# Optimization experiments

Measured on AMD Instinct MI355X. Metric: run time of the kernel, lower is better.

## Reference

```python
import jax, jax.numpy as jnp
import numpy as np

N = 100000   # nodes
E = 1600000  # edges
G = 256      # graphs in batch
IN = 128     # in_feats
H = 64       # h_feats


def _xavier(k, shape):
    fan_in, fan_out = shape
    lim = float(np.sqrt(6.0 / (fan_in + fan_out)))
    return jax.random.uniform(k, shape, jnp.float32, -lim, lim)


def setup_inputs() -> dict:
    key = jax.random.key(0)
    ks = jax.random.split(key, 12)
    x = jax.random.normal(ks[0], (N, IN), jnp.float32)
    src = jax.random.randint(ks[1], (E,), 0, N)
    dst = jax.random.randint(ks[2], (E,), 0, N)
    ew = jax.random.uniform(ks[3], (E,), jnp.float32)
    gid = jnp.sort(jax.random.randint(ks[4], (N,), 0, G))
    def lin(k, fi, fo):
        kw, kb = jax.random.split(k)
        lim = float(np.sqrt(1.0 / fi))
        return (jax.random.uniform(kw, (fi, fo), jnp.float32, -lim, lim),
                jax.random.uniform(kb, (fo,), jnp.float32, -lim, lim))
    W1 = _xavier(ks[5], (IN, H)); b1 = jnp.zeros((H,), jnp.float32)
    W2 = _xavier(ks[6], (H, H));  b2 = jnp.zeros((H,), jnp.float32)
    W3 = _xavier(ks[7], (H, H));  b3 = jnp.zeros((H,), jnp.float32)
    Dw1, Db1 = lin(ks[8], H, 16)
    Dw2, Db2 = lin(ks[9], 16, 8)
    Dw3, Db3 = lin(ks[10], 8, 1)
    return {"x": x, "src": src, "dst": dst, "ew": ew, "gid": gid,
            "W1": W1, "b1": b1, "W2": W2, "b2": b2, "W3": W3, "b3": b3,
            "Dw1": Dw1, "Db1": Db1, "Dw2": Dw2, "Db2": Db2, "Dw3": Dw3, "Db3": Db3}


def reference(x, src, dst, ew, gid, W1, b1, W2, b2, W3, b3,
              Dw1, Db1, Dw2, Db2, Dw3, Db3):
    n = x.shape[0]
    # DGL GraphConv norm='both': unweighted degrees, clamped to >= 1
    deg_out = jnp.zeros((n,), x.dtype).at[src].add(1.0)
    deg_in = jnp.zeros((n,), x.dtype).at[dst].add(1.0)
    ns = jax.lax.rsqrt(jnp.maximum(deg_out, 1.0))  # src-side norm
    nd = jax.lax.rsqrt(jnp.maximum(deg_in, 1.0))   # dst-side norm

    def conv(h, W, b):
        # apply weight first (in >= out), then gather-scale-scatter
        h = (h * ns[:, None]) @ W                      # [N, out]
        m = h[src] * ew[:, None]                       # [E, out] edge messages
        agg = jnp.zeros((n, W.shape[1]), h.dtype).at[dst].add(m)
        return agg * nd[:, None] + b

    h = jax.nn.relu(conv(x, W1, b1))
    h = jax.nn.relu(conv(h, W2, b2))
    h = jax.nn.relu(conv(h, W3, b3))

    # mean_nodes: per-graph mean pooling
    counts = jnp.zeros((G,), h.dtype).at[gid].add(1.0)
    pooled = jnp.zeros((G, h.shape[1]), h.dtype).at[gid].add(h)
    pooled = pooled / jnp.maximum(counts, 1.0)[:, None]

    h = jax.nn.relu(pooled @ Dw1 + Db1)
    h = jax.nn.relu(h @ Dw2 + Db2)
    return jax.nn.sigmoid(h @ Dw3 + Db3)  # [G, 1]
```

## Files before the change

kernel.cpp:

```cpp
#include <hip/hip_runtime.h>
#include <math.h>

#define N_NODES 100000
#define N_EDGES 1600000
#define G_GRAPHS 256
#define IN_F 128
#define H_F 64

#define HB 40
#define HCHUNK (N_EDGES / HB)
#define NWORDS (N_NODES / 4)
#define HNODES 25000
#define HWORDS (HNODES / 4)
#define HR 4

#define NREG 160
#define REG_NODES 625
#define BUCKET_CAP 11000
#define BSPAN 6400
#define NB_BUCKET (N_EDGES / BSPAN)

typedef unsigned int uint_t;
typedef unsigned short ushort_t;
typedef unsigned char uchar_t;
typedef __attribute__((ext_vector_type(8))) short short8;
typedef __attribute__((ext_vector_type(4))) float floatx4;
typedef __attribute__((ext_vector_type(2))) float floatx2;

constexpr int WROW_F = H_F + 8;

__device__ __forceinline__ ushort_t f2bf(float f) {
  uint_t u = __float_as_uint(f);
  uint_t r = (u + 0x7fffu + ((u >> 16) & 1u)) >> 16;
  return (ushort_t)r;
}
__device__ __forceinline__ float bflo(uint_t u) { return __uint_as_float(u << 16); }
__device__ __forceinline__ uchar_t f2fp8(float f) {
  return (uchar_t)(__builtin_amdgcn_cvt_pk_fp8_f32(f, f, 0, false) & 0xff);
}

__global__ __launch_bounds__(256) void build_a_kernel(
    const int* __restrict__ src, const int* __restrict__ dst,
    const float* __restrict__ ew, int* __restrict__ bcnt,
    uint2* __restrict__ bucket, uint_t* __restrict__ p8src) {
  __shared__ uint_t shm[BSPAN + 2 * NREG];
  if (blockIdx.x < NB_BUCKET) {
    uint_t* rl = shm;
    int* cnt = (int*)(shm + BSPAN);
    int* cur = cnt + NREG;
    const int e0 = blockIdx.x * BSPAN;

    for (int i = threadIdx.x; i < NREG; i += 256) cnt[i] = 0;
    __syncthreads();

    for (int i = threadIdx.x; i < BSPAN; i += 256) {
      uint_t d = (uint_t)dst[e0 + i];
      uint_t r = d / REG_NODES;
      uint_t loc = d - r * REG_NODES;
      rl[i] = (r << 16) | loc;
      atomicAdd(&cnt[r], 1);
    }
    __syncthreads();

    for (int i = threadIdx.x; i < NREG; i += 256)
      cur[i] = atomicAdd(&bcnt[i], cnt[i]);
    __syncthreads();

    for (int i = threadIdx.x; i < BSPAN; i += 256) {
      uint_t v = rl[i];
      uint_t r = v >> 16, loc = v & 0xffffu;
      int pos = atomicAdd(&cur[r], 1);
      if (pos < BUCKET_CAP)
        bucket[(size_t)r * BUCKET_CAP + pos] = make_uint2(
            (loc << 17) | (uint_t)src[e0 + i], __float_as_uint(ew[e0 + i]));
    }
  } else {
    uint_t* h = shm;
    const int idx = blockIdx.x - NB_BUCKET;
    const int r = idx / HB;
    const int b = idx % HB;
    const uint_t rbase = (uint_t)(r * HNODES);

    for (int i = threadIdx.x; i < HWORDS; i += 256) h[i] = 0u;
    __syncthreads();

    const uint4* k4 = (const uint4*)(src + b * HCHUNK);
    for (int i = threadIdx.x; i < HCHUNK / 4; i += 256) {
      uint4 v = k4[i];
      uint_t t;
      t = v.x - rbase; if (t < (uint_t)HNODES) atomicAdd(&h[t >> 2], 1u << ((t & 3u) * 8u));
      t = v.y - rbase; if (t < (uint_t)HNODES) atomicAdd(&h[t >> 2], 1u << ((t & 3u) * 8u));
      t = v.z - rbase; if (t < (uint_t)HNODES) atomicAdd(&h[t >> 2], 1u << ((t & 3u) * 8u));
      t = v.w - rbase; if (t < (uint_t)HNODES) atomicAdd(&h[t >> 2], 1u << ((t & 3u) * 8u));
    }
    __syncthreads();

    uint_t* outp = p8src + (size_t)b * NWORDS + r * HWORDS;
    for (int i = threadIdx.x; i < HWORDS; i += 256) outp[i] = h[i];
  }
}

__global__ __launch_bounds__(1024) void build_b_kernel(
    const uint2* __restrict__ bucket, const int* __restrict__ bcnt,
    const uint_t* __restrict__ p8src, uint_t* __restrict__ csr,
    int2* __restrict__ rc, float* __restrict__ nd, float* __restrict__ ns) {
  __shared__ uint_t staged[BUCKET_CAP];
  __shared__ int cnt[REG_NODES];
  __shared__ int sc[REG_NODES];
  __shared__ int ts[1024];
  const int tid = threadIdx.x;
  if (blockIdx.x >= NREG) {
    int w = (blockIdx.x - NREG) * 1024 + tid;
    if (w >= NWORDS) return;
    int c0 = 0, c1 = 0, c2 = 0, c3 = 0;
    for (int b = 0; b < HB; ++b) {
      uint_t xv = p8src[(size_t)b * NWORDS + w];
      c0 += (int)(xv & 0xffu);
      c1 += (int)((xv >> 8) & 0xffu);
      c2 += (int)((xv >> 16) & 0xffu);
      c3 += (int)((xv >> 24) & 0xffu);
    }
    ((float4*)ns)[w] = make_float4(
        rsqrtf(fmaxf((float)c0, 1.0f)), rsqrtf(fmaxf((float)c1, 1.0f)),
        rsqrtf(fmaxf((float)c2, 1.0f)), rsqrtf(fmaxf((float)c3, 1.0f)));
    return;
  }
  const int r = blockIdx.x;
  const int nE = min(bcnt[r], BUCKET_CAP);

  ts[tid] = (tid < NREG) ? min(bcnt[tid], BUCKET_CAP) : 0;
  for (int i = tid; i < REG_NODES; i += 1024) cnt[i] = 0;
  __syncthreads();
  for (int off = 1; off < 256; off <<= 1) {
    int t = (tid >= off) ? ts[tid - off] : 0;
    __syncthreads();
    ts[tid] += t;
    __syncthreads();
  }
  const int csr_base = (r == 0) ? 0 : ts[r - 1];
  __syncthreads();

  const uint2* bk = bucket + (size_t)r * BUCKET_CAP;
  for (int i = tid; i < nE; i += 1024) atomicAdd(&cnt[bk[i].x >> 17], 1);
  __syncthreads();

  int cv = (tid < REG_NODES) ? cnt[tid] : 0;
  ts[tid] = cv;
  __syncthreads();
  for (int off = 1; off < 1024; off <<= 1) {
    int t = (tid >= off) ? ts[tid - off] : 0;
    __syncthreads();
    ts[tid] += t;
    __syncthreads();
  }
  if (tid < REG_NODES) {
    int run = (tid == 0) ? 0 : ts[tid - 1];
    sc[tid] = run;
    int v = r * REG_NODES + tid;
    rc[v] = make_int2(csr_base + run, cv);
    nd[v] = rsqrtf(fmaxf((float)cv, 1.0f));
  }
  __syncthreads();

  for (int i = tid; i < nE; i += 1024) {
    uint2 e = bk[i];
    uint_t loc = e.x >> 17;
    int pos = atomicAdd(&sc[loc], 1);
    staged[pos] = ((uint_t)(f2bf(__uint_as_float(e.y)) & 0x7fff) << 17) |
                  (e.x & 0x1ffffu);
  }
  __syncthreads();

  for (int i = tid; i < nE; i += 1024) csr[csr_base + i] = staged[i];
}

template <int K, bool AFP32>
__global__ __launch_bounds__(256) void gemm_mfma_kernel(
    const void* __restrict__ Xin, const float* __restrict__ W,
    const float* __restrict__ ns, uchar_t* __restrict__ T, int ntiles) {
  constexpr int CH = K / 32;
  constexpr int WROW = K + 8;
  __shared__ __align__(16) ushort_t Wt[64 * WROW];
  const int tid = threadIdx.x;

  for (int i = tid; i < K * 64; i += 256) {
    int k = i >> 6, nn = i & 63;
    Wt[nn * WROW + k] = f2bf(W[i]);
  }
  __syncthreads();

  const int wave = tid >> 6;
  const int lane = tid & 63;
  const int tile = blockIdx.x * 4 + wave;
  if (tile >= ntiles) return;
  const int m = lane & 15;
  const int q = lane >> 4;
  const int node0 = tile * 16;

  short8 afrag[CH];
  if (AFP32) {
    const float* xr = (const float*)Xin + (size_t)(node0 + m) * K + q * 8;
#pragma unroll
    for (int c = 0; c < CH; ++c) {
      float4 xa = *(const float4*)(xr + c * 32);
      float4 xb = *(const float4*)(xr + c * 32 + 4);
      short8 a;
      a[0] = (short)f2bf(xa.x); a[1] = (short)f2bf(xa.y);
      a[2] = (short)f2bf(xa.z); a[3] = (short)f2bf(xa.w);
      a[4] = (short)f2bf(xb.x); a[5] = (short)f2bf(xb.y);
      a[6] = (short)f2bf(xb.z); a[7] = (short)f2bf(xb.w);
      afrag[c] = a;
    }
  } else {
    const ushort_t* xr = (const ushort_t*)Xin + (size_t)(node0 + m) * K + q * 8;
#pragma unroll
    for (int c = 0; c < CH; ++c)
      afrag[c] = *(const short8*)(xr + c * 32);
  }

  floatx4 acc[4];
#pragma unroll
  for (int t = 0; t < 4; ++t) acc[t] = (floatx4){0.f, 0.f, 0.f, 0.f};

#pragma unroll
  for (int t = 0; t < 4; ++t) {
    const ushort_t* wr = &Wt[(t * 16 + m) * WROW + q * 8];
#pragma unroll
    for (int c = 0; c < CH; ++c) {
      short8 bfrag = *(const short8*)(wr + c * 32);
      acc[t] = __builtin_amdgcn_mfma_f32_16x16x32_bf16(afrag[c], bfrag, acc[t], 0, 0, 0);
    }
  }

  float4 nsv = *(const float4*)(ns + node0 + q * 4);
  const float nsa[4] = {nsv.x, nsv.y, nsv.z, nsv.w};
#pragma unroll
  for (int t = 0; t < 4; ++t) {
#pragma unroll
    for (int r = 0; r < 4; ++r) {
      int node = node0 + q * 4 + r;
      T[(size_t)node * 64 + t * 16 + m] = f2fp8(acc[t][r] * nsa[r]);
    }
  }
}

__device__ __forceinline__ void ld_e8(const uint_t* __restrict__ c, int k,
                                      uint_t e[8]) {
#pragma unroll
  for (int j = 0; j < 8; ++j) e[j] = c[k + j];
}
__device__ __forceinline__ void ld_p8(const uchar_t* __restrict__ T, int l,
                                      const uint_t e[8], uint2 p[8]) {
#pragma unroll
  for (int j = 0; j < 8; ++j)
    p[j] = *((const uint2*)(T + (size_t)(e[j] & 0x1ffffu) * 64) + l);
}
__device__ __forceinline__ void gacc1(float acc[8], uint_t e, uint2 p) {
  float w = __uint_as_float((e >> 17) << 16);
  floatx2 a;
  a = __builtin_amdgcn_cvt_pk_f32_fp8(p.x, false);
  acc[0] = fmaf(a.x, w, acc[0]); acc[1] = fmaf(a.y, w, acc[1]);
  a = __builtin_amdgcn_cvt_pk_f32_fp8(p.x, true);
  acc[2] = fmaf(a.x, w, acc[2]); acc[3] = fmaf(a.y, w, acc[3]);
  a = __builtin_amdgcn_cvt_pk_f32_fp8(p.y, false);
  acc[4] = fmaf(a.x, w, acc[4]); acc[5] = fmaf(a.y, w, acc[5]);
  a = __builtin_amdgcn_cvt_pk_f32_fp8(p.y, true);
  acc[6] = fmaf(a.x, w, acc[6]); acc[7] = fmaf(a.y, w, acc[7]);
}
__device__ __forceinline__ void gacc8(float acc[8], const uint_t e[8],
                                      const uint2 p[8]) {
#pragma unroll
  for (int j = 0; j < 8; ++j) gacc1(acc, e[j], p[j]);
}
__device__ __forceinline__ void ld_e4(const uint_t* __restrict__ c, int k,
                                      uint_t e[4]) {
#pragma unroll
  for (int j = 0; j < 4; ++j) e[j] = c[k + j];
}
__device__ __forceinline__ void ld_p4(const uchar_t* __restrict__ T, int l,
                                      const uint_t e[4], uint2 p[4]) {
#pragma unroll
  for (int j = 0; j < 4; ++j)
    p[j] = *((const uint2*)(T + (size_t)(e[j] & 0x1ffffu) * 64) + l);
}
__device__ __forceinline__ void gacc4(float acc[8], const uint_t e[4],
                                      const uint2 p[4]) {
#pragma unroll
  for (int j = 0; j < 4; ++j) gacc1(acc, e[j], p[j]);
}

__device__ __forceinline__ void hs_store(ushort_t* Hs, int row, int l,
                                         const float acc[8], float ndv,
                                         float4 b0, float4 b1v) {
  uint4 ov;
  ov.x = (uint_t)f2bf(fmaxf(fmaf(acc[0], ndv, b0.x), 0.f)) |
         ((uint_t)f2bf(fmaxf(fmaf(acc[1], ndv, b0.y), 0.f)) << 16);
  ov.y = (uint_t)f2bf(fmaxf(fmaf(acc[2], ndv, b0.z), 0.f)) |
         ((uint_t)f2bf(fmaxf(fmaf(acc[3], ndv, b0.w), 0.f)) << 16);
  ov.z = (uint_t)f2bf(fmaxf(fmaf(acc[4], ndv, b1v.x), 0.f)) |
         ((uint_t)f2bf(fmaxf(fmaf(acc[5], ndv, b1v.y), 0.f)) << 16);
  ov.w = (uint_t)f2bf(fmaxf(fmaf(acc[6], ndv, b1v.z), 0.f)) |
         ((uint_t)f2bf(fmaxf(fmaf(acc[7], ndv, b1v.w), 0.f)) << 16);
  *((uint4*)&Hs[row * WROW_F + l * 8]) = ov;
}

__device__ __forceinline__ void pool_acc(float* gaccF, float* pooled, int g,
                                         int g0s, int l, const float acc[8],
                                         float ndv, float4 b0, float4 b1v) {
  const float bb[8] = {b0.x, b0.y, b0.z, b0.w, b1v.x, b1v.y, b1v.z, b1v.w};
  float vals[8];
#pragma unroll
  for (int f = 0; f < 8; ++f)
    vals[f] = bflo((uint_t)f2bf(fmaxf(fmaf(acc[f], ndv, bb[f]), 0.f)));
  int gl = g - g0s;
  if (gl >= 0 && gl < 4) {
#pragma unroll
    for (int f = 0; f < 8; ++f)
      atomicAdd(&gaccF[gl * 64 + l * 8 + f], vals[f]);
  } else {
#pragma unroll
    for (int f = 0; f < 8; ++f)
      atomicAdd(&pooled[(size_t)g * 64 + l * 8 + f], vals[f]);
  }
}

template <bool POOL>
__global__ __launch_bounds__(256, 4) void fused_kernel(
    const uint_t* __restrict__ csr, const int2* __restrict__ rc,
    const uchar_t* __restrict__ T, const float* __restrict__ nd,
    const float* __restrict__ bias, const float* __restrict__ ns,
    const float* __restrict__ W, uchar_t* __restrict__ Tout,
    const int* __restrict__ gid, float* __restrict__ pooled) {
  __shared__ __align__(16) ushort_t Hs[64 * WROW_F];
  __shared__ __align__(16) ushort_t Wt[64 * WROW_F];
  __shared__ float gaccF[4 * 64];
  __shared__ int g0s;
  const int tid = threadIdx.x;
  const int node_base = blockIdx.x * 64;

  if constexpr (POOL) {
    gaccF[tid] = 0.0f;
    if (tid == 0) g0s = gid[node_base];
  } else {
    for (int i = tid; i < H_F * 64; i += 256) {
      int k = i >> 6, nn = i & 63;
      Wt[nn * WROW_F + k] = f2bf(W[i]);
    }
  }
  __syncthreads();

  const int lane = tid & 63;
  const int wv = tid >> 6;
  const int o = lane >> 3, l = lane & 7;

  const int ln = wv * 8 + o;
  const int vA = node_base + ln;
  const int vB = vA + 32;
  const bool bok = (vB < N_NODES);

  int2 rcA = rc[vA];
  int2 rcB = bok ? rc[vB] : make_int2(0, 0);
  const uint_t* cA = csr + rcA.x;
  const uint_t* cB = csr + rcB.x;
  const int cntA = rcA.y, cntB = rcB.y;

  float accA[8] = {0, 0, 0, 0, 0, 0, 0, 0};
  float accB[8] = {0, 0, 0, 0, 0, 0, 0, 0};
  int kA = 0, kB = 0;

  while ((kA + 8 <= cntA) && (kB + 8 <= cntB)) {
    uint_t eA[8], eB[8];
    uint2 pA[8], pB[8];
    ld_e8(cA, kA, eA);
    ld_e8(cB, kB, eB);
    ld_p8(T, l, eA, pA);
    ld_p8(T, l, eB, pB);
    gacc8(accA, eA, pA);
    gacc8(accB, eB, pB);
    kA += 8;
    kB += 8;
  }
  while (kA + 8 <= cntA) {
    uint_t e[8]; uint2 p[8];
    ld_e8(cA, kA, e); ld_p8(T, l, e, p); gacc8(accA, e, p); kA += 8;
  }
  while (kB + 8 <= cntB) {
    uint_t e[8]; uint2 p[8];
    ld_e8(cB, kB, e); ld_p8(T, l, e, p); gacc8(accB, e, p); kB += 8;
  }
  {
    const bool a4 = (kA + 4 <= cntA), b4 = (kB + 4 <= cntB);
    uint_t e4a[4], e4b[4];
    uint2 p4a[4], p4b[4];
    if (a4) { ld_e4(cA, kA, e4a); ld_p4(T, l, e4a, p4a); }
    if (b4) { ld_e4(cB, kB, e4b); ld_p4(T, l, e4b, p4b); }
    if (a4) { gacc4(accA, e4a, p4a); kA += 4; }
    if (b4) { gacc4(accB, e4b, p4b); kB += 4; }
  }
  for (; kA < cntA; ++kA) {
    uint_t e = cA[kA];
    uint2 p = *((const uint2*)(T + (size_t)(e & 0x1ffffu) * 64) + l);
    gacc1(accA, e, p);
  }
  for (; kB < cntB; ++kB) {
    uint_t e = cB[kB];
    uint2 p = *((const uint2*)(T + (size_t)(e & 0x1ffffu) * 64) + l);
    gacc1(accB, e, p);
  }

  const float4 b0 = *(const float4*)&bias[l * 8];
  const float4 b1v = *(const float4*)&bias[l * 8 + 4];
  const float ndA = nd[vA];
  const float ndB = bok ? nd[vB] : 0.0f;

  if constexpr (!POOL) {
    hs_store(Hs, ln, l, accA, ndA, b0, b1v);
    if (bok) hs_store(Hs, ln + 32, l, accB, ndB, b0, b1v);
  } else {
    pool_acc(gaccF, pooled, gid[vA], g0s, l, accA, ndA, b0, b1v);
    if (bok) pool_acc(gaccF, pooled, gid[vB], g0s, l, accB, ndB, b0, b1v);
  }
  __syncthreads();

  if constexpr (!POOL) {
    const int m = lane & 15, q = lane >> 4;
    const int node0 = node_base + wv * 16;
    if (node0 < N_NODES) {
      short8 afrag[2];
      const ushort_t* xr = &Hs[(wv * 16 + m) * WROW_F + q * 8];
      afrag[0] = *(const short8*)(xr);
      afrag[1] = *(const short8*)(xr + 32);

      floatx4 acc4v[4];
#pragma unroll
      for (int t = 0; t < 4; ++t) acc4v[t] = (floatx4){0.f, 0.f, 0.f, 0.f};
#pragma unroll
      for (int t = 0; t < 4; ++t) {
        const ushort_t* wr = &Wt[(t * 16 + m) * WROW_F + q * 8];
#pragma unroll
        for (int c = 0; c < 2; ++c) {
          short8 bfrag = *(const short8*)(wr + c * 32);
          acc4v[t] = __builtin_amdgcn_mfma_f32_16x16x32_bf16(afrag[c], bfrag,
                                                            acc4v[t], 0, 0, 0);
        }
      }
      float4 nsv = *(const float4*)(ns + node0 + q * 4);
      const float nsa[4] = {nsv.x, nsv.y, nsv.z, nsv.w};
#pragma unroll
      for (int t = 0; t < 4; ++t) {
#pragma unroll
        for (int r2 = 0; r2 < 4; ++r2) {
          int node = node0 + q * 4 + r2;
          Tout[(size_t)node * 64 + t * 16 + m] = f2fp8(acc4v[t][r2] * nsa[r2]);
        }
      }
    }
  } else {
    int vlast = node_base + 63;
    if (vlast >= N_NODES) vlast = N_NODES - 1;
    int span = gid[vlast] - g0s + 1;
    if (span > 4) span = 4;
    if (tid < span * 64) {
      int gl = tid >> 6, j = tid & 63;
      int g = g0s + gl;
      if (g < G_GRAPHS) {
        float vsum = gaccF[gl * 64 + j];
        if (vsum != 0.0f) atomicAdd(&pooled[(size_t)g * 64 + j], vsum);
      }
    }
  }
}

__global__ __launch_bounds__(256) void pool_mlp_kernel(
    const float* __restrict__ pooled, const int* __restrict__ gid,
    const float* __restrict__ Dw1, const float* __restrict__ Db1,
    const float* __restrict__ Dw2, const float* __restrict__ Db2,
    const float* __restrict__ Dw3, const float* __restrict__ Db3,
    float* __restrict__ out) {
  __shared__ float mean[64];
  __shared__ float h1s[16], h2s[8];
  const int g = blockIdx.x;
  int l = 0, r = N_NODES;
  while (l < r) { int m = (l + r) >> 1; if (gid[m] < g) l = m + 1; else r = m; }
  const int lo = l;
  r = N_NODES;
  while (l < r) { int m = (l + r) >> 1; if (gid[m] < g + 1) l = m + 1; else r = m; }
  const int hi = l;

  if (threadIdx.x < 64) {
    float inv = 1.0f / fmaxf((float)(hi - lo), 1.0f);
    mean[threadIdx.x] = pooled[(size_t)g * 64 + threadIdx.x] * inv;
  }
  __syncthreads();
  if (threadIdx.x < 16) {
    int o = threadIdx.x;
    float a = Db1[o];
#pragma unroll
    for (int k = 0; k < 64; ++k) a = fmaf(mean[k], Dw1[k * 16 + o], a);
    h1s[o] = fmaxf(a, 0.0f);
  }
  __syncthreads();
  if (threadIdx.x < 8) {
    int o = threadIdx.x;
    float a = Db2[o];
#pragma unroll
    for (int k = 0; k < 16; ++k) a = fmaf(h1s[k], Dw2[k * 8 + o], a);
    h2s[o] = fmaxf(a, 0.0f);
  }
  __syncthreads();
  if (threadIdx.x == 0) {
    float a = Db3[0];
#pragma unroll
    for (int k = 0; k < 8; ++k) a = fmaf(h2s[k], Dw3[k], a);
    out[g] = 1.0f / (1.0f + expf(-a));
  }
}

extern "C" void kernel_launch(void* const* d_in, const int* in_sizes, int n_in,
                              void* d_out, int out_size, void* d_ws, size_t ws_size,
                              hipStream_t stream) {
  const float* x   = (const float*)d_in[0];
  const int*   src = (const int*)  d_in[1];
  const int*   dst = (const int*)  d_in[2];
  const float* ew  = (const float*)d_in[3];
  const int*   gid = (const int*)  d_in[4];
  const float* W1  = (const float*)d_in[5];
  const float* b1  = (const float*)d_in[6];
  const float* W2  = (const float*)d_in[7];
  const float* b2  = (const float*)d_in[8];
  const float* W3  = (const float*)d_in[9];
  const float* b3  = (const float*)d_in[10];
  const float* Dw1 = (const float*)d_in[11];
  const float* Db1 = (const float*)d_in[12];
  const float* Dw2 = (const float*)d_in[13];
  const float* Db2 = (const float*)d_in[14];
  const float* Dw3 = (const float*)d_in[15];
  const float* Db3 = (const float*)d_in[16];
  float* out = (float*)d_out;

  char* ws = (char*)d_ws;
  const size_t TSZ = (size_t)N_NODES * 64;
  const size_t BUCKET_BYTES = (size_t)NREG * BUCKET_CAP * 8;
  uchar_t*  T_a   = (uchar_t*)ws;
  uchar_t*  T_b   = (uchar_t*)(ws + TSZ);
  uint2*    bucket = (uint2*)ws;
  char* p = ws + BUCKET_BYTES;
  uint_t*   csr   = (uint_t*)p;          p += (size_t)N_EDGES * 4;
  uint_t*   p8src = (uint_t*)p;          p += (size_t)HB * NWORDS * 4;
  float*    ns    = (float*)p;           p += (size_t)N_NODES * 4;
  float*    nd    = (float*)p;           p += (size_t)N_NODES * 4;
  int2*     rc    = (int2*)p;            p += (size_t)N_NODES * 8;
  int*      bcnt  = (int*)p;             p += (size_t)NREG * 4;
  float*    pooled = (float*)p;

  const int NTILES  = N_NODES / 16;
  const int NB_A    = NB_BUCKET + HR * HB;
  const int NB_B    = NREG + (NWORDS + 1023) / 1024;
  const int NB_GEMM = (NTILES + 3) / 4;
  const int NB_F    = (N_NODES + 63) / 64;

  hipMemsetAsync(bcnt, 0,
                 NREG * sizeof(int) + G_GRAPHS * H_F * sizeof(float), stream);
  build_a_kernel<<<NB_A, 256, 0, stream>>>(src, dst, ew, bcnt, bucket, p8src);
  build_b_kernel<<<NB_B, 1024, 0, stream>>>(bucket, bcnt, p8src, csr, rc, nd, ns);

  gemm_mfma_kernel<IN_F, true><<<NB_GEMM, 256, 0, stream>>>(x, W1, ns, T_a, NTILES);
  fused_kernel<false><<<NB_F, 256, 0, stream>>>(csr, rc, T_a, nd, b1, ns, W2,
                                                T_b, nullptr, nullptr);
  fused_kernel<false><<<NB_F, 256, 0, stream>>>(csr, rc, T_b, nd, b2, ns, W3,
                                                T_a, nullptr, nullptr);
  fused_kernel<true><<<NB_F, 256, 0, stream>>>(csr, rc, T_a, nd, b3, nullptr,
                                               nullptr, nullptr, gid, pooled);

  pool_mlp_kernel<<<G_GRAPHS, 256, 0, stream>>>(pooled, gid, Dw1, Db1, Dw2, Db2,
                                                Dw3, Db3, out);
}
```

Baseline: 304.3 us.

## Pad CSR rows to 4-edge groups and simplify gather loop

CSR rows are now padded to multiples of four zero-weight entries so the aggregation can read edges as uint4 and drop scalar tail loops. The fused kernel handles the two node halves in sequential passes instead of interleaving two nodes, which lowers register pressure and allows raising the occupancy hint to 6. Shared-memory tiles use an XOR swizzle instead of row padding, and POOL instances allocate no Hs/Wt. The source histogram uses 20 partial slices instead of 40. In exchange it loses per-thread two-node memory parallelism, performs some wasted padded gathers, and overflows of the fixed slack caps would silently drop edges.

```diff
diff --git a/kernel.cpp b/kernel.cpp
--- a/kernel.cpp
+++ b/kernel.cpp
@@ -7,7 +7,7 @@
 #define IN_F 128
 #define H_F 64
 
-#define HB 40
+#define HB 20
 #define HCHUNK (N_EDGES / HB)
 #define NWORDS (N_NODES / 4)
 #define HNODES 25000
@@ -19,6 +19,9 @@
 #define BUCKET_CAP 11000
 #define BSPAN 6400
 #define NB_BUCKET (N_EDGES / BSPAN)
+#define RSLACK 1280
+#define STG_CAP 12880
+#define CSR_ALLOC 1806336
 
 typedef unsigned int uint_t;
 typedef unsigned short ushort_t;
@@ -27,8 +30,6 @@
 typedef __attribute__((ext_vector_type(4))) float floatx4;
 typedef __attribute__((ext_vector_type(2))) float floatx2;
 
-constexpr int WROW_F = H_F + 8;
-
 __device__ __forceinline__ ushort_t f2bf(float f) {
   uint_t u = __float_as_uint(f);
   uint_t r = (u + 0x7fffu + ((u >> 16) & 1u)) >> 16;
@@ -37,6 +38,10 @@
 __device__ __forceinline__ float bflo(uint_t u) { return __uint_as_float(u << 16); }
 __device__ __forceinline__ uchar_t f2fp8(float f) {
   return (uchar_t)(__builtin_amdgcn_cvt_pk_fp8_f32(f, f, 0, false) & 0xff);
+}
+__device__ __forceinline__ int sw_idx(int row, int kshort) {
+  int slot = kshort >> 3;
+  return row * 64 + (((slot ^ (row & 7)) << 3) | (kshort & 7));
 }
 
 __global__ __launch_bounds__(256) void build_a_kernel(
@@ -104,7 +109,7 @@
     const uint2* __restrict__ bucket, const int* __restrict__ bcnt,
     const uint_t* __restrict__ p8src, uint_t* __restrict__ csr,
     int2* __restrict__ rc, float* __restrict__ nd, float* __restrict__ ns) {
-  __shared__ uint_t staged[BUCKET_CAP];
+  __shared__ uint_t staged[STG_CAP];
   __shared__ int cnt[REG_NODES];
   __shared__ int sc[REG_NODES];
   __shared__ int ts[1024];
@@ -127,8 +132,9 @@
   }
   const int r = blockIdx.x;
   const int nE = min(bcnt[r], BUCKET_CAP);
-
-  ts[tid] = (tid < NREG) ? min(bcnt[tid], BUCKET_CAP) : 0;
+  const int alloc_r = ((nE + 3) & ~3) + RSLACK;
+
+  ts[tid] = (tid < NREG) ? (((min(bcnt[tid], BUCKET_CAP) + 3) & ~3) + RSLACK) : 0;
   for (int i = tid; i < REG_NODES; i += 1024) cnt[i] = 0;
   __syncthreads();
   for (int off = 1; off < 256; off <<= 1) {
@@ -145,7 +151,8 @@
   __syncthreads();
 
   int cv = (tid < REG_NODES) ? cnt[tid] : 0;
-  ts[tid] = cv;
+  int pv = (cv + 3) & ~3;
+  ts[tid] = pv;
   __syncthreads();
   for (int off = 1; off < 1024; off <<= 1) {
     int t = (tid >= off) ? ts[tid - off] : 0;
@@ -161,17 +168,24 @@
     nd[v] = rsqrtf(fmaxf((float)cv, 1.0f));
   }
   __syncthreads();
+  const int ptot = min(ts[1023], STG_CAP);
+  __syncthreads();
+
+  for (int i = tid; i < ptot; i += 1024) staged[i] = 0u;
+  __syncthreads();
 
   for (int i = tid; i < nE; i += 1024) {
     uint2 e = bk[i];
     uint_t loc = e.x >> 17;
     int pos = atomicAdd(&sc[loc], 1);
-    staged[pos] = ((uint_t)(f2bf(__uint_as_float(e.y)) & 0x7fff) << 17) |
-                  (e.x & 0x1ffffu);
-  }
-  __syncthreads();
-
-  for (int i = tid; i < nE; i += 1024) csr[csr_base + i] = staged[i];
+    if (pos < STG_CAP)
+      staged[pos] = ((uint_t)(f2bf(__uint_as_float(e.y)) & 0x7fff) << 17) |
+                    (e.x & 0x1ffffu);
+  }
+  __syncthreads();
+
+  const int out_len = min(ptot, alloc_r);
+  for (int i = tid; i < out_len; i += 1024) csr[csr_base + i] = staged[i];
 }
 
 template <int K, bool AFP32>
@@ -244,17 +258,6 @@
   }
 }
 
-__device__ __forceinline__ void ld_e8(const uint_t* __restrict__ c, int k,
-                                      uint_t e[8]) {
-#pragma unroll
-  for (int j = 0; j < 8; ++j) e[j] = c[k + j];
-}
-__device__ __forceinline__ void ld_p8(const uchar_t* __restrict__ T, int l,
-                                      const uint_t e[8], uint2 p[8]) {
-#pragma unroll
-  for (int j = 0; j < 8; ++j)
-    p[j] = *((const uint2*)(T + (size_t)(e[j] & 0x1ffffu) * 64) + l);
-}
 __device__ __forceinline__ void gacc1(float acc[8], uint_t e, uint2 p) {
   float w = __uint_as_float((e >> 17) << 16);
   floatx2 a;
@@ -267,73 +270,17 @@
   a = __builtin_amdgcn_cvt_pk_f32_fp8(p.y, true);
   acc[6] = fmaf(a.x, w, acc[6]); acc[7] = fmaf(a.y, w, acc[7]);
 }
-__device__ __forceinline__ void gacc8(float acc[8], const uint_t e[8],
-                                      const uint2 p[8]) {
-#pragma unroll
-  for (int j = 0; j < 8; ++j) gacc1(acc, e[j], p[j]);
-}
-__device__ __forceinline__ void ld_e4(const uint_t* __restrict__ c, int k,
-                                      uint_t e[4]) {
-#pragma unroll
-  for (int j = 0; j < 4; ++j) e[j] = c[k + j];
-}
-__device__ __forceinline__ void ld_p4(const uchar_t* __restrict__ T, int l,
-                                      const uint_t e[4], uint2 p[4]) {
-#pragma unroll
-  for (int j = 0; j < 4; ++j)
-    p[j] = *((const uint2*)(T + (size_t)(e[j] & 0x1ffffu) * 64) + l);
-}
-__device__ __forceinline__ void gacc4(float acc[8], const uint_t e[4],
-                                      const uint2 p[4]) {
-#pragma unroll
-  for (int j = 0; j < 4; ++j) gacc1(acc, e[j], p[j]);
-}
-
-__device__ __forceinline__ void hs_store(ushort_t* Hs, int row, int l,
-                                         const float acc[8], float ndv,
-                                         float4 b0, float4 b1v) {
-  uint4 ov;
-  ov.x = (uint_t)f2bf(fmaxf(fmaf(acc[0], ndv, b0.x), 0.f)) |
-         ((uint_t)f2bf(fmaxf(fmaf(acc[1], ndv, b0.y), 0.f)) << 16);
-  ov.y = (uint_t)f2bf(fmaxf(fmaf(acc[2], ndv, b0.z), 0.f)) |
-         ((uint_t)f2bf(fmaxf(fmaf(acc[3], ndv, b0.w), 0.f)) << 16);
-  ov.z = (uint_t)f2bf(fmaxf(fmaf(acc[4], ndv, b1v.x), 0.f)) |
-         ((uint_t)f2bf(fmaxf(fmaf(acc[5], ndv, b1v.y), 0.f)) << 16);
-  ov.w = (uint_t)f2bf(fmaxf(fmaf(acc[6], ndv, b1v.z), 0.f)) |
-         ((uint_t)f2bf(fmaxf(fmaf(acc[7], ndv, b1v.w), 0.f)) << 16);
-  *((uint4*)&Hs[row * WROW_F + l * 8]) = ov;
-}
-
-__device__ __forceinline__ void pool_acc(float* gaccF, float* pooled, int g,
-                                         int g0s, int l, const float acc[8],
-                                         float ndv, float4 b0, float4 b1v) {
-  const float bb[8] = {b0.x, b0.y, b0.z, b0.w, b1v.x, b1v.y, b1v.z, b1v.w};
-  float vals[8];
-#pragma unroll
-  for (int f = 0; f < 8; ++f)
-    vals[f] = bflo((uint_t)f2bf(fmaxf(fmaf(acc[f], ndv, bb[f]), 0.f)));
-  int gl = g - g0s;
-  if (gl >= 0 && gl < 4) {
-#pragma unroll
-    for (int f = 0; f < 8; ++f)
-      atomicAdd(&gaccF[gl * 64 + l * 8 + f], vals[f]);
-  } else {
-#pragma unroll
-    for (int f = 0; f < 8; ++f)
-      atomicAdd(&pooled[(size_t)g * 64 + l * 8 + f], vals[f]);
-  }
-}
 
 template <bool POOL>
-__global__ __launch_bounds__(256, 4) void fused_kernel(
+__global__ __launch_bounds__(256, 6) void fused_kernel(
     const uint_t* __restrict__ csr, const int2* __restrict__ rc,
     const uchar_t* __restrict__ T, const float* __restrict__ nd,
     const float* __restrict__ bias, const float* __restrict__ ns,
     const float* __restrict__ W, uchar_t* __restrict__ Tout,
     const int* __restrict__ gid, float* __restrict__ pooled) {
-  __shared__ __align__(16) ushort_t Hs[64 * WROW_F];
-  __shared__ __align__(16) ushort_t Wt[64 * WROW_F];
-  __shared__ float gaccF[4 * 64];
+  __shared__ __align__(16) ushort_t Hs[POOL ? 8 : 64 * 64];
+  __shared__ __align__(16) ushort_t Wt[POOL ? 8 : 64 * 64];
+  __shared__ float gaccF[POOL ? 4 * 64 : 1];
   __shared__ int g0s;
   const int tid = threadIdx.x;
   const int node_base = blockIdx.x * 64;
@@ -344,7 +291,7 @@
   } else {
     for (int i = tid; i < H_F * 64; i += 256) {
       int k = i >> 6, nn = i & 63;
-      Wt[nn * WROW_F + k] = f2bf(W[i]);
+      Wt[sw_idx(nn, k)] = f2bf(W[i]);
     }
   }
   __syncthreads();
@@ -352,73 +299,79 @@
   const int lane = tid & 63;
   const int wv = tid >> 6;
   const int o = lane >> 3, l = lane & 7;
-
-  const int ln = wv * 8 + o;
-  const int vA = node_base + ln;
-  const int vB = vA + 32;
-  const bool bok = (vB < N_NODES);
-
-  int2 rcA = rc[vA];
-  int2 rcB = bok ? rc[vB] : make_int2(0, 0);
-  const uint_t* cA = csr + rcA.x;
-  const uint_t* cB = csr + rcB.x;
-  const int cntA = rcA.y, cntB = rcB.y;
-
-  float accA[8] = {0, 0, 0, 0, 0, 0, 0, 0};
-  float accB[8] = {0, 0, 0, 0, 0, 0, 0, 0};
-  int kA = 0, kB = 0;
-
-  while ((kA + 8 <= cntA) && (kB + 8 <= cntB)) {
-    uint_t eA[8], eB[8];
-    uint2 pA[8], pB[8];
-    ld_e8(cA, kA, eA);
-    ld_e8(cB, kB, eB);
-    ld_p8(T, l, eA, pA);
-    ld_p8(T, l, eB, pB);
-    gacc8(accA, eA, pA);
-    gacc8(accB, eB, pB);
-    kA += 8;
-    kB += 8;
-  }
-  while (kA + 8 <= cntA) {
-    uint_t e[8]; uint2 p[8];
-    ld_e8(cA, kA, e); ld_p8(T, l, e, p); gacc8(accA, e, p); kA += 8;
-  }
-  while (kB + 8 <= cntB) {
-    uint_t e[8]; uint2 p[8];
-    ld_e8(cB, kB, e); ld_p8(T, l, e, p); gacc8(accB, e, p); kB += 8;
-  }
-  {
-    const bool a4 = (kA + 4 <= cntA), b4 = (kB + 4 <= cntB);
-    uint_t e4a[4], e4b[4];
-    uint2 p4a[4], p4b[4];
-    if (a4) { ld_e4(cA, kA, e4a); ld_p4(T, l, e4a, p4a); }
-    if (b4) { ld_e4(cB, kB, e4b); ld_p4(T, l, e4b, p4b); }
-    if (a4) { gacc4(accA, e4a, p4a); kA += 4; }
-    if (b4) { gacc4(accB, e4b, p4b); kB += 4; }
-  }
-  for (; kA < cntA; ++kA) {
-    uint_t e = cA[kA];
-    uint2 p = *((const uint2*)(T + (size_t)(e & 0x1ffffu) * 64) + l);
-    gacc1(accA, e, p);
-  }
-  for (; kB < cntB; ++kB) {
-    uint_t e = cB[kB];
-    uint2 p = *((const uint2*)(T + (size_t)(e & 0x1ffffu) * 64) + l);
-    gacc1(accB, e, p);
-  }
+  const uint2* Tp = (const uint2*)T;
 
   const float4 b0 = *(const float4*)&bias[l * 8];
   const float4 b1v = *(const float4*)&bias[l * 8 + 4];
-  const float ndA = nd[vA];
-  const float ndB = bok ? nd[vB] : 0.0f;
-
-  if constexpr (!POOL) {
-    hs_store(Hs, ln, l, accA, ndA, b0, b1v);
-    if (bok) hs_store(Hs, ln + 32, l, accB, ndB, b0, b1v);
-  } else {
-    pool_acc(gaccF, pooled, gid[vA], g0s, l, accA, ndA, b0, b1v);
-    if (bok) pool_acc(gaccF, pooled, gid[vB], g0s, l, accB, ndB, b0, b1v);
+
+#pragma unroll 1
+  for (int pass = 0; pass < 2; ++pass) {
+    const int ln = pass * 32 + wv * 8 + o;
+    const int v = node_base + ln;
+    if (v < N_NODES) {
+      int2 rcv = rc[v];
+      const uint4* c4 = (const uint4*)(csr + rcv.x);
+      const int nb4 = (rcv.y + 3) >> 2;
+
+      float acc[8] = {0, 0, 0, 0, 0, 0, 0, 0};
+      int kq = 0;
+      for (; kq + 2 <= nb4; kq += 2) {
+        uint4 ea = c4[kq];
+        uint4 eb = c4[kq + 1];
+        uint2 p0 = Tp[(size_t)(ea.x & 0x1ffffu) * 8 + l];
+        uint2 p1 = Tp[(size_t)(ea.y & 0x1ffffu) * 8 + l];
+        uint2 p2 = Tp[(size_t)(ea.z & 0x1ffffu) * 8 + l];
+        uint2 p3 = Tp[(size_t)(ea.w & 0x1ffffu) * 8 + l];
+        uint2 p4 = Tp[(size_t)(eb.x & 0x1ffffu) * 8 + l];
+        uint2 p5 = Tp[(size_t)(eb.y & 0x1ffffu) * 8 + l];
+        uint2 p6 = Tp[(size_t)(eb.z & 0x1ffffu) * 8 + l];
+        uint2 p7 = Tp[(size_t)(eb.w & 0x1ffffu) * 8 + l];
+        gacc1(acc, ea.x, p0); gacc1(acc, ea.y, p1);
+        gacc1(acc, ea.z, p2); gacc1(acc, ea.w, p3);
+        gacc1(acc, eb.x, p4); gacc1(acc, eb.y, p5);
+        gacc1(acc, eb.z, p6); gacc1(acc, eb.w, p7);
+      }
+      if (kq < nb4) {
+        uint4 ea = c4[kq];
+        uint2 p0 = Tp[(size_t)(ea.x & 0x1ffffu) * 8 + l];
+        uint2 p1 = Tp[(size_t)(ea.y & 0x1ffffu) * 8 + l];
+        uint2 p2 = Tp[(size_t)(ea.z & 0x1ffffu) * 8 + l];
+        uint2 p3 = Tp[(size_t)(ea.w & 0x1ffffu) * 8 + l];
+        gacc1(acc, ea.x, p0); gacc1(acc, ea.y, p1);
+        gacc1(acc, ea.z, p2); gacc1(acc, ea.w, p3);
+      }
+
+      const float ndv = nd[v];
+      if constexpr (!POOL) {
+        uint4 ov;
+        ov.x = (uint_t)f2bf(fmaxf(fmaf(acc[0], ndv, b0.x), 0.f)) |
+               ((uint_t)f2bf(fmaxf(fmaf(acc[1], ndv, b0.y), 0.f)) << 16);
+        ov.y = (uint_t)f2bf(fmaxf(fmaf(acc[2], ndv, b0.z), 0.f)) |
+               ((uint_t)f2bf(fmaxf(fmaf(acc[3], ndv, b0.w), 0.f)) << 16);
+        ov.z = (uint_t)f2bf(fmaxf(fmaf(acc[4], ndv, b1v.x), 0.f)) |
+               ((uint_t)f2bf(fmaxf(fmaf(acc[5], ndv, b1v.y), 0.f)) << 16);
+        ov.w = (uint_t)f2bf(fmaxf(fmaf(acc[6], ndv, b1v.z), 0.f)) |
+               ((uint_t)f2bf(fmaxf(fmaf(acc[7], ndv, b1v.w), 0.f)) << 16);
+        *((uint4*)&Hs[sw_idx(ln, l * 8)]) = ov;
+      } else {
+        const float bb[8] = {b0.x, b0.y, b0.z, b0.w, b1v.x, b1v.y, b1v.z, b1v.w};
+        float vals[8];
+#pragma unroll
+        for (int f = 0; f < 8; ++f)
+          vals[f] = bflo((uint_t)f2bf(fmaxf(fmaf(acc[f], ndv, bb[f]), 0.f)));
+        int g = gid[v];
+        int gl = g - g0s;
+        if (gl >= 0 && gl < 4) {
+#pragma unroll
+          for (int f = 0; f < 8; ++f)
+            atomicAdd(&gaccF[gl * 64 + l * 8 + f], vals[f]);
+        } else {
+#pragma unroll
+          for (int f = 0; f < 8; ++f)
+            atomicAdd(&pooled[(size_t)g * 64 + l * 8 + f], vals[f]);
+        }
+      }
+    }
   }
   __syncthreads();
 
@@ -427,19 +380,17 @@
     const int node0 = node_base + wv * 16;
     if (node0 < N_NODES) {
       short8 afrag[2];
-      const ushort_t* xr = &Hs[(wv * 16 + m) * WROW_F + q * 8];
-      afrag[0] = *(const short8*)(xr);
-      afrag[1] = *(const short8*)(xr + 32);
+      afrag[0] = *(const short8*)&Hs[sw_idx(wv * 16 + m, q * 8)];
+      afrag[1] = *(const short8*)&Hs[sw_idx(wv * 16 + m, q * 8 + 32)];
 
       floatx4 acc4v[4];
 #pragma unroll
       for (int t = 0; t < 4; ++t) acc4v[t] = (floatx4){0.f, 0.f, 0.f, 0.f};
 #pragma unroll
       for (int t = 0; t < 4; ++t) {
-        const ushort_t* wr = &Wt[(t * 16 + m) * WROW_F + q * 8];
 #pragma unroll
         for (int c = 0; c < 2; ++c) {
-          short8 bfrag = *(const short8*)(wr + c * 32);
+          short8 bfrag = *(const short8*)&Wt[sw_idx(t * 16 + m, q * 8 + c * 32)];
           acc4v[t] = __builtin_amdgcn_mfma_f32_16x16x32_bf16(afrag[c], bfrag,
                                                             acc4v[t], 0, 0, 0);
         }
@@ -545,7 +496,7 @@
   uchar_t*  T_b   = (uchar_t*)(ws + TSZ);
   uint2*    bucket = (uint2*)ws;
   char* p = ws + BUCKET_BYTES;
-  uint_t*   csr   = (uint_t*)p;          p += (size_t)N_EDGES * 4;
+  uint_t*   csr   = (uint_t*)p;          p += (size_t)CSR_ALLOC * 4;
   uint_t*   p8src = (uint_t*)p;          p += (size_t)HB * NWORDS * 4;
   float*    ns    = (float*)p;           p += (size_t)N_NODES * 4;
   float*    nd    = (float*)p;           p += (size_t)N_NODES * 4;
```

After: 289.2 us. 4.9% less time.
